# Kernel tuning notes

Hardware: AMD Instinct MI355X
Metric: run time of the kernel (lower is better)

## Reference

```python
import jax, jax.numpy as jnp
import numpy as np

B, S, D, H = 2, 2048, 2048, 16
DH = D // H  # 128
EPS = 1e-6


def _rms_norm(x, w):
    # RMSNorm over last dim with learnable scale
    var = jnp.mean(jnp.square(x), axis=-1, keepdims=True)
    return x * jax.lax.rsqrt(var + EPS) * w


def _apply_rope(x, angles):
    # x: [B, S, H, DH]; angles: [S, DH//2]; interleaved pair rotation
    xs = x.reshape(*x.shape[:-1], DH // 2, 2)
    x0, x1 = xs[..., 0], xs[..., 1]
    cos = jnp.cos(angles)[None, :, None, :]  # [1,S,1,DH/2]
    sin = jnp.sin(angles)[None, :, None, :]
    r0 = x0 * cos - x1 * sin
    r1 = x0 * sin + x1 * cos
    return jnp.stack([r0, r1], axis=-1).reshape(x.shape)


def setup_inputs() -> dict:
    key = jax.random.key(0)
    ks = jax.random.split(key, 4)
    x = jax.random.normal(ks[0], (B, S, D), dtype=jnp.float32)
    # standard RoPE angle table: pos * inv_freq
    inv_freq = 1.0 / (10000.0 ** (jnp.arange(0, DH, 2, dtype=jnp.float32) / DH))
    pos = jnp.arange(S, dtype=jnp.float32)
    rp_freqs = pos[:, None] * inv_freq[None, :]  # [S, DH/2]
    Win = jax.random.normal(ks[1], (3 * D, D), dtype=jnp.float32) * (D ** -0.5)
    b_in = jnp.zeros((3 * D,), dtype=jnp.float32)
    Wout = jax.random.normal(ks[2], (D, D), dtype=jnp.float32) * (D ** -0.5)
    b_out = jnp.zeros((D,), dtype=jnp.float32)
    qk_w = jnp.ones((DH,), dtype=jnp.float32)
    out_w = jnp.ones((D,), dtype=jnp.float32)
    return {"x": x, "rp_freqs": rp_freqs, "Win": Win, "b_in": b_in,
            "Wout": Wout, "b_out": b_out, "qk_w": qk_w, "out_w": out_w}


def reference(x, rp_freqs, Win, b_in, Wout, b_out, qk_w, out_w):
    b, s, d = x.shape
    qkv = jnp.einsum('bsd,ed->bse', x, Win) + b_in  # [B,S,3D]
    qkv = qkv.reshape(b, s, 3, H, DH)
    q, k, v = qkv[:, :, 0], qkv[:, :, 1], qkv[:, :, 2]  # each [B,S,H,DH]
    q = _apply_rope(q, rp_freqs)
    k = _apply_rope(k, rp_freqs)
    q = _rms_norm(q, qk_w)
    k = _rms_norm(k, qk_w)
    # causal SDPA, scale = 1/sqrt(DH) (default)
    a = jax.nn.dot_product_attention(q, k, v, is_causal=True)  # [B,S,H,DH]
    a = a.reshape(b, s, d)
    a = _rms_norm(a, out_w)
    return jnp.einsum('bsd,ed->bse', a, Wout) + b_out
```

## Files before the change

### kernel.cpp

```cpp
#include <hip/hip_runtime.h>
#include <cstdint>
#include <cstddef>

#define Bq  2
#define Sq  2048
#define Dq  2048
#define Hq  16
#define DHq 128
#define E3q 6144

typedef __attribute__((ext_vector_type(8))) short s16x8;
typedef __attribute__((ext_vector_type(4))) float f32x4;

__device__ __forceinline__ unsigned short f2bf(float f){
  union { float f; unsigned u; } v; v.f = f;
  unsigned r = v.u + 0x7FFFu + ((v.u >> 16) & 1u);
  return (unsigned short)(r >> 16);
}
__device__ __forceinline__ float bf2f(unsigned short b){
  union { unsigned u; float f; } v; v.u = ((unsigned)b) << 16;
  return v.f;
}
__device__ __forceinline__ unsigned cvtpk_bf16(float lo, float hi){
  unsigned r;
  asm("v_cvt_pk_bf16_f32 %0, %1, %2" : "=v"(r) : "v"(lo), "v"(hi));
  return r;
}

__device__ __forceinline__ void gload_lds16(const void* g, void* l){
  __builtin_amdgcn_global_load_lds(
      (const __attribute__((address_space(1))) void*)g,
      (__attribute__((address_space(3))) void*)l, 16, 0, 0);
}

__global__ __launch_bounds__(256) void k_convert(const float* __restrict__ in,
                                                 unsigned short* __restrict__ out, int n4){
  int stride = gridDim.x * blockDim.x;
  for (int i = blockIdx.x*blockDim.x + threadIdx.x; i < n4; i += stride){
    float4 v = reinterpret_cast<const float4*>(in)[i];
    ushort4 o;
    o.x = f2bf(v.x); o.y = f2bf(v.y); o.z = f2bf(v.z); o.w = f2bf(v.w);
    reinterpret_cast<ushort4*>(out)[i] = o;
  }
}

template<int F32OUT>
__global__ __launch_bounds__(512, 1) void k_gemm_bt(const unsigned short* __restrict__ A,
                                                    const unsigned short* __restrict__ Bt,
                                                    const float* __restrict__ bias,
                                                    void* __restrict__ C,
                                                    int M, int N, int K, int gx){
  const int nwg = gridDim.x;
  const int cpx = nwg >> 3;
  const int bid = blockIdx.x;
  const int swz = (bid & 7) * cpx + (bid >> 3);
  const int by = swz / gx, bx = swz - by*gx;
  const int m0 = by * 128, n0 = bx * 256;

  const int tid = threadIdx.x;
  const int w = tid >> 6, lane = tid & 63, g = lane >> 4, c = lane & 15;
  const int wm = w >> 2, wn = w & 3;

  __shared__ __align__(16) unsigned short L[4 * 12288];

  const int NT = K >> 5;

  const int arow = tid >> 2, apc = tid & 3;
  const int brow0 = tid >> 2, bpc0 = tid & 3;
  const int brow1 = (tid + 512) >> 2, bpc1 = tid & 3;
  const unsigned short* Abase = &A [(size_t)(m0 + arow )*K + (size_t)((apc ^ ((arow >>1)&3))*8)];
  const unsigned short* Bbase0 = &Bt[(size_t)(n0 + brow0)*K + (size_t)((bpc0 ^ ((brow0>>1)&3))*8)];
  const unsigned short* Bbase1 = &Bt[(size_t)(n0 + brow1)*K + (size_t)((bpc1 ^ ((brow1>>1)&3))*8)];

  auto stage = [&](int tile, int slot){
    const int kt = tile << 5;
    unsigned short* Ls = &L[slot * 12288];
    gload_lds16(Abase  + kt, &Ls[tid*8]);
    gload_lds16(Bbase0 + kt, &Ls[4096 + tid*8]);
    gload_lds16(Bbase1 + kt, &Ls[4096 + (tid+512)*8]);
  };

  f32x4 acc[4][4];
#pragma unroll
  for (int i=0;i<4;i++)
#pragma unroll
    for (int j=0;j<4;j++)
#pragma unroll
      for (int r=0;r<4;r++) acc[i][j][r] = 0.f;

  int aoff[4], boff[4];
#pragma unroll
  for (int mi=0;mi<4;mi++){
    int row = wm*64 + mi*16 + c;
    aoff[mi] = row*32 + ((g ^ ((row>>1)&3)) << 3);
  }
#pragma unroll
  for (int ni=0;ni<4;ni++){
    int row = wn*64 + ni*16 + c;
    boff[ni] = 4096 + row*32 + ((g ^ ((row>>1)&3)) << 3);
  }

  stage(0, 0); stage(1, 1); stage(2, 2);

  for (int t = 0; t < NT; ++t){
    if (t < NT-2)      { asm volatile("s_waitcnt vmcnt(6)" ::: "memory"); }
    else if (t == NT-2){ asm volatile("s_waitcnt vmcnt(3)" ::: "memory"); }
    else               { asm volatile("s_waitcnt vmcnt(0)" ::: "memory"); }
    __builtin_amdgcn_s_barrier();
    __builtin_amdgcn_sched_barrier(0);
    if (t+3 < NT) stage(t+3, (t+3)&3);

    const unsigned short* Ls = &L[(t&3) * 12288];
    s16x8 bfr[4];
#pragma unroll
    for (int ni=0;ni<4;ni++) bfr[ni] = *(const s16x8*)&Ls[boff[ni]];
    __builtin_amdgcn_s_setprio(1);
#pragma unroll
    for (int mi=0;mi<4;mi++){
      s16x8 af = *(const s16x8*)&Ls[aoff[mi]];
#pragma unroll
      for (int ni=0;ni<4;ni++)
        acc[mi][ni] = __builtin_amdgcn_mfma_f32_16x16x32_bf16(af, bfr[ni], acc[mi][ni], 0,0,0);
    }
    __builtin_amdgcn_s_setprio(0);
  }

#pragma unroll
  for (int ni=0;ni<4;ni++){
    const int col = n0 + wn*64 + ni*16 + c;
    const float bv = bias[col];
#pragma unroll
    for (int mi=0;mi<4;mi++){
      const int row = m0 + wm*64 + mi*16 + g*4;
#pragma unroll
      for (int r=0;r<4;r++){
        float v = acc[mi][ni][r] + bv;
        if (F32OUT) ((float*)C)[(size_t)(row+r)*N + col] = v;
        else ((unsigned short*)C)[(size_t)(row+r)*N + col] = f2bf(v);
      }
    }
  }
}

__global__ __launch_bounds__(256) void k_rope_qk(const unsigned short* __restrict__ QKV,
                                                 const float* __restrict__ rp,
                                                 const float* __restrict__ qk_w,
                                                 unsigned short* __restrict__ Qp,
                                                 unsigned short* __restrict__ Kp){
  const int p = threadIdx.x;
  const int s = blockIdx.x*4 + threadIdx.y;
  const int h = blockIdx.y;
  const int b = blockIdx.z;
  const size_t n = (size_t)b*Sq + s;
  const int bh = b*Hq + h;

  float ang = rp[s*64 + p];
  float sn, cs; sincosf(ang, &sn, &cs);
  float w0 = qk_w[2*p], w1 = qk_w[2*p+1];
  const float QSCALE = 0.08838834764831845f * 1.4426950408889634f;

  {
    unsigned q01 = *(const unsigned*)&QKV[n*E3q + h*DHq + 2*p];
    float x0 = bf2f((unsigned short)(q01 & 0xFFFFu));
    float x1 = bf2f((unsigned short)(q01 >> 16));
    float r0 = x0*cs - x1*sn, r1 = x0*sn + x1*cs;
    float ss = r0*r0 + r1*r1;
#pragma unroll
    for (int m=1;m<64;m<<=1) ss += __shfl_xor(ss, m);
    float sc = rsqrtf(ss/128.f + 1e-6f) * QSCALE;
    unsigned short o0 = f2bf(r0*sc*w0), o1 = f2bf(r1*sc*w1);
    *(unsigned*)&Qp[((size_t)bh*Sq + s)*DHq + 2*p] = (unsigned)o0 | ((unsigned)o1<<16);
  }
  {
    unsigned k01 = *(const unsigned*)&QKV[n*E3q + Dq + h*DHq + 2*p];
    float x0 = bf2f((unsigned short)(k01 & 0xFFFFu));
    float x1 = bf2f((unsigned short)(k01 >> 16));
    float r0 = x0*cs - x1*sn, r1 = x0*sn + x1*cs;
    float ss = r0*r0 + r1*r1;
#pragma unroll
    for (int m=1;m<64;m<<=1) ss += __shfl_xor(ss, m);
    float sc = rsqrtf(ss/128.f + 1e-6f);
    unsigned short o0 = f2bf(r0*sc*w0), o1 = f2bf(r1*sc*w1);
    *(unsigned*)&Kp[((size_t)bh*Sq + s)*DHq + 2*p] = (unsigned)o0 | ((unsigned)o1<<16);
  }
}

__global__ __launch_bounds__(256) void k_transpose_v(const unsigned short* __restrict__ QKV,
                                                     unsigned short* __restrict__ Vt){
  const int sblk = blockIdx.x;
  const int bh = blockIdx.y;
  const int b = bh >> 4, h = bh & 15;
  const int tid = threadIdx.x;
  __shared__ unsigned short T[128][136];

  const size_t base = ((size_t)(b*Sq) + sblk*128) * E3q + 2*(size_t)Dq + h*DHq;
#pragma unroll
  for (int i=0;i<8;i++){
    int pk = tid + i*256;
    int row = pk >> 4, cc = (pk & 15) * 8;
    s16x8 v = *(const s16x8*)&QKV[base + (size_t)row*E3q + cc];
    *(s16x8*)&T[row][cc] = v;
  }
  __syncthreads();
  const int dh = tid >> 1, sh = (tid & 1) * 64;
  unsigned short buf[64];
#pragma unroll
  for (int s=0;s<64;s++) buf[s] = T[sh + s][dh];
  size_t obase = ((size_t)bh*DHq + dh)*Sq + sblk*128 + sh;
#pragma unroll
  for (int i=0;i<8;i++)
    *(s16x8*)&Vt[obase + i*8] = *(const s16x8*)&buf[i*8];
}

__global__ __launch_bounds__(256, 2) void k_attn(const unsigned short* __restrict__ Qp,
                                                 const unsigned short* __restrict__ Kp,
                                                 const unsigned short* __restrict__ Vt,
                                                 unsigned short* __restrict__ Ar){
  const int L = blockIdx.x;
  int bh, qtile;
  if (L < 256){ bh = L >> 3; qtile = 8 + (L & 7); }
  else { int Ml = L - 256; bh = Ml >> 3; qtile = 7 - (Ml & 7); }
  const int b = bh >> 4, h = bh & 15;
  const int tid = threadIdx.x;
  const int w = tid >> 6, lane = tid & 63, g = lane >> 4, c = lane & 15;
  const int r0w = qtile*128 + w*32;

  const unsigned short* Qh = Qp + (size_t)bh * Sq * DHq;
  const unsigned short* Kh = Kp + (size_t)bh * Sq * DHq;
  const unsigned short* Vh = Vt + (size_t)bh * DHq * Sq;

  __shared__ __align__(16) unsigned short Ks[2][64*128];
  __shared__ __align__(16) unsigned short Vs[2][128*64];
  __shared__ __align__(16) unsigned short Pl[4][32*64];
  unsigned short* Pw = &Pl[w][0];

  s16x8 qf[2][4];
#pragma unroll
  for (int mi=0;mi<2;mi++)
#pragma unroll
    for (int kc=0;kc<4;kc++)
      qf[mi][kc] = *(const s16x8*)&Qh[(size_t)(r0w + mi*16 + c)*DHq + kc*32 + g*8];

  f32x4 acc[2][8];
#pragma unroll
  for (int mi=0;mi<2;mi++)
#pragma unroll
    for (int dt=0;dt<8;dt++)
#pragma unroll
      for (int r=0;r<4;r++) acc[mi][dt][r] = 0.f;
  float m_r[2] = { -INFINITY, -INFINITY };
  float l_p[2] = { 0.f, 0.f };

  const int nsteps = 2*qtile + 2;

  auto stage = [&](int j0s, int bufi){
#pragma unroll
    for (int i=0;i<4;i++){
      int pk = tid + i*256;
      int row = pk>>4, pc = pk&15;
      gload_lds16(&Kh[(size_t)(j0s+row)*DHq + ((pc^(row&7))<<3)], &Ks[bufi][pk*8]);
    }
#pragma unroll
    for (int i=0;i<4;i++){
      int pk = tid + i*256;
      int row = pk>>3, pc = pk&7;
      gload_lds16(&Vh[(size_t)row*Sq + j0s + ((pc^(row&7))<<3)], &Vs[bufi][pk*8]);
    }
  };

  stage(0, 0);
  __syncthreads();

  for (int t=0; t<nsteps; ++t){
    const int j0 = t*64;
    if (t+1 < nsteps) stage((t+1)*64, (t+1)&1);

    if (j0 <= r0w + 31){
      const unsigned short* Kc = &Ks[t&1][0];
      const unsigned short* Vc = &Vs[t&1][0];

      f32x4 sv[2][4];
#pragma unroll
      for (int mi=0;mi<2;mi++)
#pragma unroll
        for (int js=0;js<4;js++)
#pragma unroll
          for (int r=0;r<4;r++) sv[mi][js][r] = 0.f;

      __builtin_amdgcn_s_setprio(1);
#pragma unroll
      for (int js=0;js<4;js++){
        s16x8 kf[4];
#pragma unroll
        for (int kc=0;kc<4;kc++)
          kf[kc] = *(const s16x8*)&Kc[(js*16 + c)*128 + (((kc*4+g)^(c&7))<<3)];
#pragma unroll
        for (int mi=0;mi<2;mi++)
#pragma unroll
          for (int kc=0;kc<4;kc++)
            sv[mi][js] = __builtin_amdgcn_mfma_f32_16x16x32_bf16(kf[kc], qf[mi][kc], sv[mi][js], 0,0,0);
      }
      __builtin_amdgcn_s_setprio(0);

      if (j0 + 63 > r0w){
#pragma unroll
        for (int mi=0;mi<2;mi++){
          const int q = r0w + mi*16 + c;
#pragma unroll
          for (int js=0;js<4;js++)
#pragma unroll
            for (int r=0;r<4;r++)
              if (j0 + js*16 + g*4 + r > q) sv[mi][js][r] = -INFINITY;
        }
      }

      float pmx[2];
#pragma unroll
      for (int mi=0;mi<2;mi++){
        float mx = fmaxf(fmaxf(sv[mi][0][0],sv[mi][0][1]), fmaxf(sv[mi][0][2],sv[mi][0][3]));
#pragma unroll
        for (int js=1;js<4;js++){
          float a = fmaxf(fmaxf(sv[mi][js][0],sv[mi][js][1]), fmaxf(sv[mi][js][2],sv[mi][js][3]));
          mx = fmaxf(mx, a);
        }
        mx = fmaxf(mx, __shfl_xor(mx, 16));
        mx = fmaxf(mx, __shfl_xor(mx, 32));
        pmx[mi] = mx;
      }
      int need = (pmx[0] > m_r[0] + 8.f) | (pmx[1] > m_r[1] + 8.f);
      if (__any(need)){
#pragma unroll
        for (int mi=0;mi<2;mi++){
          float mnew = fmaxf(m_r[mi], pmx[mi]);
          float corr = exp2f(m_r[mi] - mnew);
          l_p[mi] *= corr;
          m_r[mi] = mnew;
#pragma unroll
          for (int dt=0;dt<8;dt++)
#pragma unroll
            for (int r=0;r<4;r++) acc[mi][dt][r] *= corr;
        }
      }
#pragma unroll
      for (int mi=0;mi<2;mi++){
        const float mm = m_r[mi];
        const int rowoff = (mi*16 + c)*64;
#pragma unroll
        for (int js=0;js<4;js++){
          float e0 = exp2f(sv[mi][js][0] - mm);
          float e1 = exp2f(sv[mi][js][1] - mm);
          float e2 = exp2f(sv[mi][js][2] - mm);
          float e3 = exp2f(sv[mi][js][3] - mm);
          l_p[mi] += (e0+e1)+(e2+e3);
          uint2 pk2;
          pk2.x = cvtpk_bf16(e0, e1);
          pk2.y = cvtpk_bf16(e2, e3);
          const int kc8 = js*2 + (g>>1);
          *(uint2*)&Pw[rowoff + ((kc8 ^ (c&7))<<3) + (g&1)*4] = pk2;
        }
      }

      s16x8 pfr[2][2];
#pragma unroll
      for (int mi=0;mi<2;mi++)
#pragma unroll
        for (int kc=0;kc<2;kc++)
          pfr[mi][kc] = *(const s16x8*)&Pw[(mi*16 + c)*64 + (((kc*4+g)^(c&7))<<3)];
      __builtin_amdgcn_s_setprio(1);
#pragma unroll
      for (int dt=0; dt<8; dt++){
#pragma unroll
        for (int kc=0;kc<2;kc++){
          s16x8 vfr = *(const s16x8*)&Vc[(dt*16 + c)*64 + (((kc*4+g)^(c&7))<<3)];
#pragma unroll
          for (int mi=0;mi<2;mi++)
            acc[mi][dt] = __builtin_amdgcn_mfma_f32_16x16x32_bf16(vfr, pfr[mi][kc], acc[mi][dt], 0,0,0);
        }
      }
      __builtin_amdgcn_s_setprio(0);
    }
    __syncthreads();
  }

#pragma unroll
  for (int mi=0;mi<2;mi++){
    float l = l_p[mi];
    l += __shfl_xor(l, 16);
    l += __shfl_xor(l, 32);
    const float inv = 1.f / l;
    const int row = r0w + mi*16 + c;
    unsigned short* dst = &Ar[((size_t)(b*Sq + row))*Dq + h*DHq];
#pragma unroll
    for (int dt=0; dt<8; dt++){
      uint2 o2;
      o2.x = cvtpk_bf16(acc[mi][dt][0]*inv, acc[mi][dt][1]*inv);
      o2.y = cvtpk_bf16(acc[mi][dt][2]*inv, acc[mi][dt][3]*inv);
      *(uint2*)&dst[dt*16 + g*4] = o2;
    }
  }
}

__global__ __launch_bounds__(256) void k_rmsnorm(unsigned short* __restrict__ A,
                                                 const float* __restrict__ w){
  const int row = blockIdx.x;
  const int tid = threadIdx.x;
  s16x8 v = *(const s16x8*)&A[(size_t)row*Dq + tid*8];
  float f[8]; float ss = 0.f;
#pragma unroll
  for (int i=0;i<8;i++){ f[i] = bf2f((unsigned short)v[i]); ss += f[i]*f[i]; }
#pragma unroll
  for (int m=1;m<64;m<<=1) ss += __shfl_xor(ss, m);
  __shared__ float red[4];
  if ((tid&63)==0) red[tid>>6] = ss;
  __syncthreads();
  ss = red[0]+red[1]+red[2]+red[3];
  float sc = rsqrtf(ss/2048.f + 1e-6f);
  unsigned short o[8];
#pragma unroll
  for (int i=0;i<8;i++) o[i] = f2bf(f[i]*sc*w[tid*8+i]);
  *(s16x8*)&A[(size_t)row*Dq + tid*8] = *(const s16x8*)o;
}

extern "C" void kernel_launch(void* const* d_in, const int* in_sizes, int n_in,
                              void* d_out, int out_size, void* d_ws, size_t ws_size,
                              hipStream_t stream){
  const float* x     = (const float*)d_in[0];
  const float* rp    = (const float*)d_in[1];
  const float* Win   = (const float*)d_in[2];
  const float* b_in  = (const float*)d_in[3];
  const float* Wout  = (const float*)d_in[4];
  const float* b_out = (const float*)d_in[5];
  const float* qk_w  = (const float*)d_in[6];
  const float* out_w = (const float*)d_in[7];
  float* outp = (float*)d_out;

  if (ws_size < (160ull<<20)) return;

  char* ws = (char*)d_ws;
  unsigned short* Xb    = (unsigned short*)(ws);
  unsigned short* Wb    = (unsigned short*)(ws + (16ull<<20));
  unsigned short* Woutb = (unsigned short*)(ws + (40ull<<20));
  unsigned short* QKVb  = (unsigned short*)(ws + (48ull<<20));
  unsigned short* Qp    = (unsigned short*)(ws + (96ull<<20));
  unsigned short* Kp    = (unsigned short*)(ws + (112ull<<20));
  unsigned short* Vt    = (unsigned short*)(ws + (128ull<<20));
  unsigned short* Ar    = (unsigned short*)(ws + (144ull<<20));

  k_convert<<<2048, 256, 0, stream>>>(x,    Xb,    (Bq*Sq*Dq)/4);
  k_convert<<<2048, 256, 0, stream>>>(Win,  Wb,    (E3q*Dq)/4);
  k_convert<<<1024, 256, 0, stream>>>(Wout, Woutb, (Dq*Dq)/4);
  k_gemm_bt<0><<<768, 512, 0, stream>>>(Xb, Wb, b_in, QKVb, Bq*Sq, E3q, Dq, E3q/256);
  k_rope_qk<<<dim3(Sq/4, Hq, Bq), dim3(64,4), 0, stream>>>(QKVb, rp, qk_w, Qp, Kp);
  k_transpose_v<<<dim3(Sq/128, Bq*Hq), 256, 0, stream>>>(QKVb, Vt);
  k_attn<<<512, 256, 0, stream>>>(Qp, Kp, Vt, Ar);
  k_rmsnorm<<<Bq*Sq, 256, 0, stream>>>(Ar, out_w);
  k_gemm_bt<1><<<256, 512, 0, stream>>>(Ar, Woutb, b_out, outp, Bq*Sq, Dq, Dq, Dq/256);
}
```

Before: 303.2 us.

## Deepen GEMM LDS pipeline to six stages and remap tiles per XCD

The bf16 GEMM kernel's shared-memory ring grows from 4 to 6 slots and prefetches 5 tiles ahead, with waitcnt thresholds adjusted to match, so more global loads are in flight and load latency is hidden better. The block-to-tile mapping also changes: each XCD now owns a fixed group of 4 row blocks and walks across column tiles, which is meant to improve L2 reuse of the A rows within an XCD. LDS use rises to 144KB per block. The new mapping assumes M/128 = 32 rows, which holds for both launches here but is hardcoded.

```diff
diff --git a/kernel.cpp b/kernel.cpp
--- a/kernel.cpp
+++ b/kernel.cpp
@@ -49,26 +49,25 @@
                                                     const unsigned short* __restrict__ Bt,
                                                     const float* __restrict__ bias,
                                                     void* __restrict__ C,
-                                                    int M, int N, int K, int gx){
-  const int nwg = gridDim.x;
-  const int cpx = nwg >> 3;
+                                                    int M, int N, int K){
   const int bid = blockIdx.x;
-  const int swz = (bid & 7) * cpx + (bid >> 3);
-  const int by = swz / gx, bx = swz - by*gx;
+  const int xcd = bid & 7, u = bid >> 3;
+  const int by = xcd*4 + (u & 3);
+  const int bx = u >> 2;
   const int m0 = by * 128, n0 = bx * 256;
 
   const int tid = threadIdx.x;
   const int w = tid >> 6, lane = tid & 63, g = lane >> 4, c = lane & 15;
   const int wm = w >> 2, wn = w & 3;
 
-  __shared__ __align__(16) unsigned short L[4 * 12288];
+  __shared__ __align__(16) unsigned short L[6 * 12288];
 
   const int NT = K >> 5;
 
   const int arow = tid >> 2, apc = tid & 3;
   const int brow0 = tid >> 2, bpc0 = tid & 3;
   const int brow1 = (tid + 512) >> 2, bpc1 = tid & 3;
-  const unsigned short* Abase = &A [(size_t)(m0 + arow )*K + (size_t)((apc ^ ((arow >>1)&3))*8)];
+  const unsigned short* Abase  = &A [(size_t)(m0 + arow )*K + (size_t)((apc ^ ((arow >>1)&3))*8)];
   const unsigned short* Bbase0 = &Bt[(size_t)(n0 + brow0)*K + (size_t)((bpc0 ^ ((brow0>>1)&3))*8)];
   const unsigned short* Bbase1 = &Bt[(size_t)(n0 + brow1)*K + (size_t)((bpc1 ^ ((brow1>>1)&3))*8)];
 
@@ -100,17 +99,21 @@
     boff[ni] = 4096 + row*32 + ((g ^ ((row>>1)&3)) << 3);
   }
 
-  stage(0, 0); stage(1, 1); stage(2, 2);
-
+  stage(0,0); stage(1,1); stage(2,2); stage(3,3); stage(4,4);
+
+  int slot = 0;
   for (int t = 0; t < NT; ++t){
-    if (t < NT-2)      { asm volatile("s_waitcnt vmcnt(6)" ::: "memory"); }
-    else if (t == NT-2){ asm volatile("s_waitcnt vmcnt(3)" ::: "memory"); }
-    else               { asm volatile("s_waitcnt vmcnt(0)" ::: "memory"); }
+    const int rem = NT-1-t;
+    if (rem >= 4)      asm volatile("s_waitcnt vmcnt(12)" ::: "memory");
+    else if (rem == 3) asm volatile("s_waitcnt vmcnt(9)"  ::: "memory");
+    else if (rem == 2) asm volatile("s_waitcnt vmcnt(6)"  ::: "memory");
+    else if (rem == 1) asm volatile("s_waitcnt vmcnt(3)"  ::: "memory");
+    else               asm volatile("s_waitcnt vmcnt(0)"  ::: "memory");
     __builtin_amdgcn_s_barrier();
     __builtin_amdgcn_sched_barrier(0);
-    if (t+3 < NT) stage(t+3, (t+3)&3);
-
-    const unsigned short* Ls = &L[(t&3) * 12288];
+    if (t+5 < NT) stage(t+5, slot == 0 ? 5 : slot-1);
+
+    const unsigned short* Ls = &L[slot * 12288];
     s16x8 bfr[4];
 #pragma unroll
     for (int ni=0;ni<4;ni++) bfr[ni] = *(const s16x8*)&Ls[boff[ni]];
@@ -123,6 +126,7 @@
         acc[mi][ni] = __builtin_amdgcn_mfma_f32_16x16x32_bf16(af, bfr[ni], acc[mi][ni], 0,0,0);
     }
     __builtin_amdgcn_s_setprio(0);
+    slot = (slot == 5) ? 0 : slot+1;
   }
 
 #pragma unroll
@@ -449,10 +453,10 @@
   k_convert<<<2048, 256, 0, stream>>>(x,    Xb,    (Bq*Sq*Dq)/4);
   k_convert<<<2048, 256, 0, stream>>>(Win,  Wb,    (E3q*Dq)/4);
   k_convert<<<1024, 256, 0, stream>>>(Wout, Woutb, (Dq*Dq)/4);
-  k_gemm_bt<0><<<768, 512, 0, stream>>>(Xb, Wb, b_in, QKVb, Bq*Sq, E3q, Dq, E3q/256);
+  k_gemm_bt<0><<<768, 512, 0, stream>>>(Xb, Wb, b_in, QKVb, Bq*Sq, E3q, Dq);
   k_rope_qk<<<dim3(Sq/4, Hq, Bq), dim3(64,4), 0, stream>>>(QKVb, rp, qk_w, Qp, Kp);
   k_transpose_v<<<dim3(Sq/128, Bq*Hq), 256, 0, stream>>>(QKVb, Vt);
   k_attn<<<512, 256, 0, stream>>>(Qp, Kp, Vt, Ar);
   k_rmsnorm<<<Bq*Sq, 256, 0, stream>>>(Ar, out_w);
-  k_gemm_bt<1><<<256, 512, 0, stream>>>(Ar, Woutb, b_out, outp, Bq*Sq, Dq, Dq, Dq/256);
-}
+  k_gemm_bt<1><<<256, 512, 0, stream>>>(Ar, Woutb, b_out, outp, Bq*Sq, Dq, Dq);
+}
```

New measurement: 300.1 us. No clear change (-1.0%).
